# Kernel optimization log

Hardware: AMD Instinct MI355X
Metric: run time of the kernel (lower is better)

## Reference

```python
import jax, jax.numpy as jnp
import numpy as np

HID, H, C, L = 128, 4, 128, 3  # hidden, heads, per-head out (concat=False -> mean over heads), layers
OUT = 256
N_HEX, N_VERT, N_EDGE, B = 19, 54, 72, 1024
F_HEX, F_VERT, F_EDGE, F_PLY = 9, 7, 5, 14


def _topology():
    # Deterministic stand-in for the Catan board topology (same edge counts as the env).
    rng = np.random.RandomState(0)
    hv = rng.randint(0, N_VERT, size=(N_HEX, 6))            # each hex touches 6 vertices
    v0 = rng.randint(0, N_VERT, size=N_EDGE)                # board-edge endpoints
    v1 = (v0 + 1 + rng.randint(0, N_VERT - 1, size=N_EDGE)) % N_VERT
    h_src = np.repeat(np.arange(N_HEX), 6); h_dst = hv.reshape(-1)           # 114 edges
    e_src = np.repeat(np.arange(N_EDGE), 2); e_dst = np.stack([v0, v1], 1).reshape(-1)  # 144
    vv_s = np.concatenate([v0, v1]); vv_d = np.concatenate([v1, v0])          # 144
    # (src_idx, dst_idx, n_dst) per relation, order matches RELATION_TYPES
    rels = [(h_src, h_dst, N_VERT),   # hex -> vertex
            (h_dst, h_src, N_HEX),    # vertex -> hex
            (e_dst, e_src, N_EDGE),   # vertex -> edge
            (e_src, e_dst, N_VERT),   # edge -> vertex
            (vv_s, vv_d, N_VERT)]     # vertex -> vertex
    return [(jnp.asarray(s, jnp.int32), jnp.asarray(d, jnp.int32), nd) for s, d, nd in rels]

RELS = _topology()
REL_TYPES = [("hex", "vertex"), ("vertex", "hex"), ("vertex", "edge"), ("edge", "vertex"), ("vertex", "vertex")]
NODE_TYPES = ("hex", "vertex", "edge")


def _gat(x_src, x_dst, W, a_s, a_d, b, src, dst, n_dst):
    """PyG GATConv (heads=H, concat=False, add_self_loops=False, shared lin)."""
    bsz = x_src.shape[0]
    g = (x_src @ W).reshape(bsz, -1, H, C)    # [B,Ns,H,C]
    gd = (x_dst @ W).reshape(bsz, -1, H, C)   # [B,Nd,H,C]
    es = jnp.einsum('bnhc,hc->bnh', g, a_s)
    ed = jnp.einsum('bnhc,hc->bnh', gd, a_d)
    e = jax.nn.leaky_relu(es[:, src] + ed[:, dst], 0.2)   # [B,E,H]
    e = jnp.transpose(e, (1, 0, 2))                       # [E,B,H]
    m = jax.ops.segment_max(e, dst, num_segments=n_dst)   # per-dst softmax
    ex = jnp.exp(e - m[dst])
    s = jax.ops.segment_sum(ex, dst, num_segments=n_dst)
    alpha = ex / (s[dst] + 1e-16)
    msg = jnp.transpose(g, (1, 0, 2, 3))[src] * alpha[..., None]   # [E,B,H,C]
    out = jax.ops.segment_sum(msg, dst, num_segments=n_dst)       # [Nd,B,H,C]
    return jnp.transpose(out.mean(axis=2), (1, 0, 2)) + b         # mean over heads, + bias


def _ln(x, g, b):
    mu = x.mean(-1, keepdims=True)
    var = ((x - mu) ** 2).mean(-1, keepdims=True)
    return (x - mu) / jnp.sqrt(var + 1e-5) * g + b


def setup_inputs() -> dict:
    key = jax.random.key(0)
    ks = jax.random.split(key, 20)
    rn = lambda k, shape, s=0.05: jax.random.normal(k, shape, jnp.float32) * s
    pool_dim = 3 * HID + F_PLY
    return {
        'hex_features': rn(ks[0], (B, N_HEX, F_HEX), 1.0),
        'vertex_features': rn(ks[1], (B, N_VERT, F_VERT), 1.0),
        'edge_features': rn(ks[2], (B, N_EDGE, F_EDGE), 1.0),
        'player_features': rn(ks[3], (B, 4, F_PLY), 1.0),
        'in_hexW': rn(ks[4], (F_HEX, HID)), 'in_hexb': jnp.zeros((HID,), jnp.float32),
        'in_vertW': rn(ks[5], (F_VERT, HID)), 'in_vertb': jnp.zeros((HID,), jnp.float32),
        'in_edgeW': rn(ks[6], (F_EDGE, HID)), 'in_edgeb': jnp.zeros((HID,), jnp.float32),
        'gat_W': rn(ks[7], (L, 5, HID, H * C)),
        'gat_asrc': rn(ks[8], (L, 5, H, C)),
        'gat_adst': rn(ks[9], (L, 5, H, C)),
        'gat_b': jnp.zeros((L, 5, C), jnp.float32),
        'ln_g': jnp.ones((L, 3, HID), jnp.float32),
        'ln_b': jnp.zeros((L, 3, HID), jnp.float32),
        'mlp_W1': rn(ks[10], (pool_dim, HID)), 'mlp_b1': jnp.zeros((HID,), jnp.float32),
        'mlp_W2': rn(ks[11], (HID, OUT)), 'mlp_b2': jnp.zeros((OUT,), jnp.float32),
        'current_player': jax.random.randint(ks[12], (B,), 0, 4, jnp.int32),
    }


def reference(hex_features, vertex_features, edge_features, player_features,
              in_hexW, in_hexb, in_vertW, in_vertb, in_edgeW, in_edgeb,
              gat_W, gat_asrc, gat_adst, gat_b, ln_g, ln_b,
              mlp_W1, mlp_b1, mlp_W2, mlp_b2, current_player):
    x = {'hex': hex_features @ in_hexW + in_hexb,
         'vertex': vertex_features @ in_vertW + in_vertb,
         'edge': edge_features @ in_edgeW + in_edgeb}
    for l in range(L):
        agg = {nt: jnp.zeros_like(x[nt]) for nt in NODE_TYPES}
        for r, (st, dt) in enumerate(REL_TYPES):
            src, dst, n_dst = RELS[r]
            agg[dt] = agg[dt] + _gat(x[st], x[dt], gat_W[l, r], gat_asrc[l, r],
                                     gat_adst[l, r], gat_b[l, r], src, dst, n_dst)
        for i, nt in enumerate(NODE_TYPES):
            x[nt] = jax.nn.relu(_ln(agg[nt] + x[nt], ln_g[l, i], ln_b[l, i]))
    pools = [x[nt].mean(axis=1) for nt in NODE_TYPES]  # mean-pool each node type
    cur = jnp.take_along_axis(player_features, current_player[:, None, None], axis=1)[:, 0]
    feat = jnp.concatenate(pools + [cur], axis=-1)     # [B, 3*HID + F_PLY]
    h = jax.nn.relu(feat @ mlp_W1 + mlp_b1)
    return h @ mlp_W2 + mlp_b2
```

## Files before the change

### kernel.cpp

```cpp
#include <hip/hip_runtime.h>
#include <math.h>

#define NB 1024
#define NHEX 19
#define NVERT 54
#define NEDGE 72
#define NNODE 145
#define HID 128
#define NLAYERS 3
#define MAXE 144
#define OUTD 256
#define FPLY 14
#define POOLD 398

typedef unsigned short ushort_t;
typedef short bf16x8 __attribute__((ext_vector_type(8)));
typedef float f32x4 __attribute__((ext_vector_type(4)));
typedef float f32x2 __attribute__((ext_vector_type(2)));

static __device__ __forceinline__ float bf2f(ushort_t u) {
    return __uint_as_float(((unsigned int)u) << 16);
}
static __device__ __forceinline__ ushort_t f2bf(float f) {
    unsigned int u = __float_as_uint(f);
    return (ushort_t)((u + 0x7fffu + ((u >> 16) & 1u)) >> 16);
}
static __device__ __forceinline__ unsigned pk2(float lo, float hi) {
    unsigned r;
    asm("v_cvt_pk_bf16_f32 %0, %1, %2" : "=v"(r) : "v"(lo), "v"(hi));
    return r;
}
static __device__ __forceinline__ float blo(unsigned u) { return __uint_as_float(u << 16); }
static __device__ __forceinline__ float bhi(unsigned u) { return __uint_as_float(u & 0xffff0000u); }
static __device__ __forceinline__ f32x4 MF(uint4 a, uint4 b, f32x4 c) {
    return __builtin_amdgcn_mfma_f32_16x16x32_bf16(
        __builtin_bit_cast(bf16x8, a), __builtin_bit_cast(bf16x8, b), c, 0, 0, 0);
}

__device__ __forceinline__ void topo_body(int* __restrict__ cst_g, unsigned* __restrict__ pck_g) {
    __shared__ unsigned mt[624];
    __shared__ int t6[624];
    __shared__ int sc[624];
    __shared__ int hv[114], v0a[72], v1a[72];
    __shared__ int cnt[80];
    __shared__ int dloc[73 * 24];
    __shared__ int J186;
    const int tid = threadIdx.x;

    if (tid == 0) {
        unsigned s = 0u;
        for (int i = 0; i < 624; ++i) { mt[i] = s; s = 1812433253u * (s ^ (s >> 30)) + (unsigned)i + 1u; }
    }
    __syncthreads();
    {
        unsigned a = 0, bb = 0, c = 0;
        if (tid < 227) { a = mt[tid]; bb = mt[tid + 1]; c = mt[tid + 397]; }
        __syncthreads();
        if (tid < 227) {
            unsigned y = (a & 0x80000000u) | (bb & 0x7fffffffu);
            mt[tid] = c ^ (y >> 1) ^ ((bb & 1u) ? 0x9908b0dfu : 0u);
        }
        __syncthreads();
    }
    {
        int i = 227 + tid;
        unsigned a = 0, bb = 0, c = 0;
        if (tid < 227) { a = mt[i]; bb = mt[i + 1]; c = mt[i - 227]; }
        __syncthreads();
        if (tid < 227) {
            unsigned y = (a & 0x80000000u) | (bb & 0x7fffffffu);
            mt[i] = c ^ (y >> 1) ^ ((bb & 1u) ? 0x9908b0dfu : 0u);
        }
        __syncthreads();
    }
    {
        int i = 454 + tid;
        unsigned a = 0, bb = 0, c = 0;
        if (tid < 170) { a = mt[i]; bb = mt[(i + 1) % 624]; c = mt[i - 227]; }
        __syncthreads();
        if (tid < 170) {
            unsigned y = (a & 0x80000000u) | (bb & 0x7fffffffu);
            mt[i] = c ^ (y >> 1) ^ ((bb & 1u) ? 0x9908b0dfu : 0u);
        }
        __syncthreads();
    }
    for (int i = tid; i < 624; i += 256) {
        unsigned y = mt[i];
        y ^= y >> 11; y ^= (y << 7) & 0x9d2c5680u; y ^= (y << 15) & 0xefc60000u; y ^= y >> 18;
        t6[i] = (int)(y & 63u);
    }
    __syncthreads();
#define SCAN624()                                                          \
    for (int off = 1; off < 624; off <<= 1) {                              \
        int v0_ = 0, v1_ = 0, v2_ = 0;                                     \
        int i0 = tid, i1 = tid + 256, i2 = tid + 512;                      \
        if (i0 >= off) v0_ = sc[i0 - off];                                 \
        if (i1 >= off) v1_ = sc[i1 - off];                                 \
        if (i2 < 624 && i2 >= off) v2_ = sc[i2 - off];                     \
        __syncthreads();                                                   \
        sc[i0] += v0_; sc[i1] += v1_;                                      \
        if (i2 < 624) sc[i2] += v2_;                                       \
        __syncthreads();                                                   \
    }
    for (int i = tid; i < 624; i += 256) sc[i] = (t6[i] <= 53) ? 1 : 0;
    __syncthreads();
    SCAN624();
    for (int i = tid; i < 624; i += 256) {
        if (t6[i] <= 53) {
            int k = sc[i];
            if (k <= 114) hv[k - 1] = t6[i];
            else if (k <= 186) v0a[k - 115] = t6[i];
            if (k == 186) J186 = i;
        }
    }
    __syncthreads();
    int Jcap = J186;
    for (int i = tid; i < 624; i += 256) sc[i] = (i > Jcap && t6[i] <= 52) ? 1 : 0;
    __syncthreads();
    SCAN624();
    for (int i = tid; i < 624; i += 256) {
        if (i > Jcap && t6[i] <= 52) {
            int k = sc[i];
            if (k <= 72) v1a[k - 1] = (v0a[k - 1] + 1 + t6[i]) % 54;
        }
    }
    __syncthreads();
#undef SCAN624
    const int En[5] = {114, 114, 144, 144, 144};
    const int Ndn[5] = {54, 19, 72, 54, 54};
    for (int r = 0; r < 5; ++r) {
        int E = En[r], Nd = Ndn[r];
        int myc = 0;
        if (tid < Nd) {
            int* ss = dloc + tid * 24;
            for (int k = 0; k < E; ++k) {
                int s, d;
                if (r == 0)      { s = k / 6; d = hv[k]; }
                else if (r == 1) { s = hv[k]; d = k / 6; }
                else if (r == 2) { s = (k & 1) ? v1a[k >> 1] : v0a[k >> 1]; d = k >> 1; }
                else if (r == 3) { s = k >> 1; d = (k & 1) ? v1a[k >> 1] : v0a[k >> 1]; }
                else             { s = (k < 72) ? v0a[k] : v1a[k - 72]; d = (k < 72) ? v1a[k] : v0a[k - 72]; }
                if (d != tid) continue;
                int f = -1;
                for (int i2 = 0; i2 < myc; ++i2) if ((ss[i2] & 255) == s) { f = i2; break; }
                if (f >= 0) ss[f] += 1 << 16;
                else { if (myc < 24) { ss[myc++] = s | (1 << 16); } }
            }
            cnt[tid] = myc;
        }
        __syncthreads();
        for (int off = 1; off < 128; off <<= 1) {
            int v = 0;
            if (tid < Nd && tid >= off) v = cnt[tid - off];
            __syncthreads();
            if (tid < Nd && tid >= off) cnt[tid] += v;
            __syncthreads();
        }
        if (tid < Nd) {
            int st = cnt[tid] - myc;
            cst_g[r * 73 + tid] = st;
            if (tid == Nd - 1) cst_g[r * 73 + Nd] = cnt[tid];
            int* ss = dloc + tid * 24;
            for (int i2 = 0; i2 < myc; ++i2)
                pck_g[r * 144 + st + i2] =
                    (unsigned)((ss[i2] & 255) | (tid << 8) | ((ss[i2] >> 16) << 16));
        }
        __syncthreads();
    }
}

__device__ __forceinline__ void wvec_body(int lr, const float* __restrict__ gat_W,
                                          const float* __restrict__ gat_asrc,
                                          const float* __restrict__ gat_adst,
                                          ushort_t* __restrict__ wvb) {
    __shared__ float as_s[512], ad_s[512];
    int tid = threadIdx.x;
    for (int i = tid; i < 512; i += 256) {
        as_s[i] = gat_asrc[(size_t)lr * 512 + i];
        ad_s[i] = gat_adst[(size_t)lr * 512 + i];
    }
    __syncthreads();
    ushort_t* wb = wvb + (size_t)lr * 2048;
    const float* W = gat_W + (size_t)lr * 128 * 512;
    int t127 = tid & 127, rhalf = tid >> 7;
    int h = t127 >> 5, c4 = t127 & 31;
    for (int k0 = 0; k0 < 128; k0 += 2) {
        int k = k0 + rhalf;
        float4 wv4 = *(const float4*)(W + (size_t)k * 512 + h * 128 + c4 * 4);
        const float* a = as_s + h * 128 + c4 * 4;
        const float* dd = ad_s + h * 128 + c4 * 4;
        float pa = wv4.x * a[0] + wv4.y * a[1] + wv4.z * a[2] + wv4.w * a[3];
        float pd = wv4.x * dd[0] + wv4.y * dd[1] + wv4.z * dd[2] + wv4.w * dd[3];
        for (int m = 1; m < 32; m <<= 1) { pa += __shfl_xor(pa, m, 64); pd += __shfl_xor(pd, m, 64); }
        if (c4 == 0) {
            ushort_t pah = f2bf(pa), pdh = f2bf(pd);
            ushort_t pal = f2bf(pa - bf2f(pah)), pdl = f2bf(pd - bf2f(pdh));
            wb[h * 128 + k] = pah;        wb[(4 + h) * 128 + k] = pdh;
            wb[(8 + h) * 128 + k] = pal;  wb[(12 + h) * 128 + k] = pdl;
        }
    }
}

__device__ __forceinline__ void wp_body(int lrh, const float* __restrict__ gat_W, ushort_t* __restrict__ Wp) {
    __shared__ ushort_t tr[128 * 130];
    int lr = lrh >> 2, h = lrh & 3;
    const float* Wsrc = gat_W + (size_t)lr * 128 * 512 + h * 128;
    for (int i = threadIdx.x; i < 128 * 32; i += 256) {
        int k = i >> 5, q = i & 31;
        float4 v = *(const float4*)(Wsrc + (size_t)k * 512 + q * 4);
        int n = q * 4;
        tr[(n + 0) * 130 + k] = f2bf(v.x);
        tr[(n + 1) * 130 + k] = f2bf(v.y);
        tr[(n + 2) * 130 + k] = f2bf(v.z);
        tr[(n + 3) * 130 + k] = f2bf(v.w);
    }
    __syncthreads();
    ushort_t* dst = Wp + (size_t)lrh * 128 * 128;
    for (int i = threadIdx.x; i < 128 * 16; i += 256) {
        int n = i >> 4, q = i & 15;
        const ushort_t* s = tr + n * 130 + q * 8;
        uint4 o;
        o.x = (unsigned)s[0] | ((unsigned)s[1] << 16);
        o.y = (unsigned)s[2] | ((unsigned)s[3] << 16);
        o.z = (unsigned)s[4] | ((unsigned)s[5] << 16);
        o.w = (unsigned)s[6] | ((unsigned)s[7] << 16);
        *(uint4*)(dst + n * 128 + q * 8) = o;
    }
}

__device__ __forceinline__ void proj_body(int b, const float* __restrict__ hexf, const float* __restrict__ vertf,
                                          const float* __restrict__ edgef,
                                          const float* __restrict__ Wh, const float* __restrict__ bh,
                                          const float* __restrict__ Wv, const float* __restrict__ bv,
                                          const float* __restrict__ We, const float* __restrict__ be,
                                          ushort_t* __restrict__ xb) {
    __shared__ float Wl[(9 + 7 + 5) * 128];
    __shared__ float bl[3 * 128];
    int tid = threadIdx.x;
    for (int i = tid; i < 9 * 128; i += 256) Wl[i] = Wh[i];
    for (int i = tid; i < 7 * 128; i += 256) Wl[9 * 128 + i] = Wv[i];
    for (int i = tid; i < 5 * 128; i += 256) Wl[16 * 128 + i] = We[i];
    if (tid < 128) { bl[tid] = bh[tid]; bl[128 + tid] = bv[tid]; bl[256 + tid] = be[tid]; }
    __syncthreads();
    int c = tid & 127;
    for (int n = tid >> 7; n < NNODE; n += 2) {
        const float* f; const float* W; const float* bias; int K;
        if (n < NHEX)              { f = hexf  + ((size_t)b * NHEX  + n) * 9;                  W = Wl;            bias = bl;       K = 9; }
        else if (n < NHEX + NVERT) { f = vertf + ((size_t)b * NVERT + (n - NHEX)) * 7;         W = Wl + 9 * 128;  bias = bl + 128; K = 7; }
        else                       { f = edgef + ((size_t)b * NEDGE + (n - NHEX - NVERT)) * 5; W = Wl + 16 * 128; bias = bl + 256; K = 5; }
        float acc = bias[c];
        for (int k = 0; k < K; ++k) acc += f[k] * W[k * 128 + c];
        xb[((size_t)b * NNODE + n) * HID + c] = f2bf(acc);
    }
}

__global__ __launch_bounds__(256) void k_pre(
        int* __restrict__ cst_g, unsigned* __restrict__ pck_g,
        const float* __restrict__ gatW, const float* __restrict__ gatas,
        const float* __restrict__ gatad, ushort_t* __restrict__ wvb, ushort_t* __restrict__ Wp,
        const float* __restrict__ hexf, const float* __restrict__ vertf, const float* __restrict__ edgef,
        const float* __restrict__ Wh, const float* __restrict__ bh,
        const float* __restrict__ Wv, const float* __restrict__ bv,
        const float* __restrict__ We, const float* __restrict__ be,
        ushort_t* __restrict__ xb) {
    unsigned kb = blockIdx.x;
    if (kb == 0)       topo_body(cst_g, pck_g);
    else if (kb < 16)  wvec_body((int)kb - 1, gatW, gatas, gatad, wvb);
    else if (kb < 76)  wp_body((int)kb - 16, gatW, Wp);
    else               proj_body((int)kb - 76, hexf, vertf, edgef, Wh, bh, Wv, bv, We, be, xb);
}

template<int KIND>
__device__ __forceinline__ void gnn_body(char* smem, int b,
        const ushort_t* __restrict__ xb_cur, ushort_t* __restrict__ xb_nxt,
        const int* __restrict__ cst_all, const unsigned* __restrict__ pck_all,
        const ushort_t* __restrict__ wvb, const ushort_t* __restrict__ Wp_g,
        const float* __restrict__ gatb_g,
        const float* __restrict__ lg, const float* __restrict__ lb, int l) {
    constexpr int ND    = (KIND == 0 ? 19 : KIND == 1 ? 72 : 54);
    constexpr int DB    = (KIND == 0 ? 0 : KIND == 1 ? 73 : 19);
    constexpr int NSMAX = (KIND == 2 ? 72 : 54);
    constexpr int NRELF = (KIND == 2 ? 3 : 1);
    constexpr int MT    = (ND + 15) / 16;
    constexpr int O_Y   = (ND + NSMAX) * 256;
    constexpr int YSZ   = (KIND == 2 ? ND * 256 : 0);
    constexpr int O_ESD = O_Y + YSZ;
    constexpr int O_AL  = O_ESD + 4032;
    constexpr int O_CST = O_AL + 2304;
    constexpr int O_PCK = O_CST + 304;

    constexpr int NS_A[3][3] = {{54, 0, 0}, {54, 0, 0}, {19, 72, 54}};
    constexpr int SB_A[3][3] = {{19, 0, 0}, {19, 0, 0}, {0, 73, 19}};
    constexpr int RR_A[3][3] = {{1, 0, 0}, {2, 0, 0}, {0, 3, 4}};

    float*    esd  = (float*)(smem + O_ESD);
    float*    alph = (float*)(smem + O_AL);
    int*      cstL = (int*)(smem + O_CST);
    unsigned* pckL = (unsigned*)(smem + O_PCK);

    const int tid = threadIdx.x, lane = tid & 63, wid = tid >> 6;
    const int nr0 = wid * 32 + (lane & 15);
    const int kc16 = (lane >> 4) * 16;
    const ushort_t* xcb = xb_cur + (size_t)b * NNODE * HID;

#define XBA(row, cb) (((row) * 256 + (cb)) ^ (((row) & 7) << 4))
#define YBA(row, cb) ((KIND == 2 ? O_Y : 0) + ((((row) * 256) + (cb)) ^ (((row) & 7) << 4)))

    for (int i = tid; i < ND * 16; i += 256) {
        int row = i >> 4, q = i & 15;
        uint4 o = *(const uint4*)(xcb + (size_t)(DB + row) * HID + q * 8);
        *(uint4*)(smem + XBA(row, q * 16)) = o;
    }

    f32x4 acc[MT][2];
#pragma unroll
    for (int mt = 0; mt < MT; ++mt) {
        acc[mt][0] = (f32x4){0.f, 0.f, 0.f, 0.f};
        acc[mt][1] = (f32x4){0.f, 0.f, 0.f, 0.f};
    }

#pragma unroll
    for (int ri = 0; ri < NRELF; ++ri) {
        const int NS = NS_A[KIND][ri], SBG = SB_A[KIND][ri], r = RR_A[KIND][ri];
        const bool SELF = (KIND == 2 && ri == 2);
        const int RL = SELF ? ND : ND + NS;
        const int lr = l * 5 + r;

        if (!SELF)
            for (int i = tid; i < NS * 16; i += 256) {
                int row = ND + (i >> 4), q = i & 15;
                uint4 o = *(const uint4*)(xcb + (size_t)(SBG + (i >> 4)) * HID + q * 8);
                *(uint4*)(smem + XBA(row, q * 16)) = o;
            }
        for (int i = tid; i <= ND; i += 256) cstL[i] = cst_all[r * 73 + i];
        for (int i = tid; i < 144; i += 256) pckL[i] = pck_all[r * 144 + i];
        __syncthreads();

        {
            const ushort_t* wv = wvb + (size_t)lr * 2048;
            uint4 bw[4];
#pragma unroll
            for (int ks = 0; ks < 4; ++ks)
                bw[ks] = *(const uint4*)(wv + (lane & 15) * 128 + ks * 32 + (lane >> 4) * 8);
            const int T = (RL + 15) >> 4;
            for (int t = wid; t < T; t += 4) {
                f32x4 e = (f32x4){0.f, 0.f, 0.f, 0.f};
                int arow = t * 16 + (lane & 15);
#pragma unroll
                for (int ks = 0; ks < 4; ++ks) {
                    uint4 av = *(const uint4*)(smem + XBA(arow, ks * 64 + kc16));
                    e = MF(av, bw[ks], e);
                }
#pragma unroll
                for (int g = 0; g < 4; ++g) {
                    float sv = e[g] + __shfl_xor(e[g], 8, 64);
                    int row = t * 16 + (lane >> 4) * 4 + g;
                    if ((lane & 15) < 8 && row < RL) esd[row * 8 + (lane & 15)] = sv;
                }
            }
        }
        __syncthreads();

        for (int i = tid; i < ND * 4; i += 256) {
            int d = i >> 2, h = i & 3;
            int s0 = cstL[d], s1 = cstL[d + 1];
            if (s0 == s1) continue;
            float edv = esd[d * 8 + 4 + h];
            float m = -1e30f;
            for (int j = s0; j < s1; ++j) {
                int s = pckL[j] & 255;
                float sv = esd[(SELF ? s : ND + s) * 8 + h] + edv;
                sv = (sv >= 0.f) ? sv : 0.2f * sv;
                alph[j * 4 + h] = sv;
                m = fmaxf(m, sv);
            }
            float sum = 0.f;
            for (int j = s0; j < s1; ++j) {
                float e = (float)(pckL[j] >> 16) * __expf(alph[j * 4 + h] - m);
                alph[j * 4 + h] = e;
                sum += e;
            }
            float inv = 1.f / (sum + 1e-16f);
            for (int j = s0; j < s1; ++j) alph[j * 4 + h] *= inv;
        }
        __syncthreads();

        for (int h = 0; h < 4; ++h) {
            for (int i = tid; i < ND * 16; i += 256) {
                int d = i >> 4, c8 = i & 15;
                int s0 = cstL[d], s1 = cstL[d + 1];
                f32x2 a01 = (f32x2){0.f, 0.f}, a23 = (f32x2){0.f, 0.f};
                f32x2 a45 = (f32x2){0.f, 0.f}, a67 = (f32x2){0.f, 0.f};
                for (int j = s0; j < s1; ++j) {
                    float al = alph[j * 4 + h];
                    f32x2 al2 = (f32x2){al, al};
                    int s = pckL[j] & 255;
                    int srow = SELF ? s : ND + s;
                    uint4 xv = *(const uint4*)(smem + XBA(srow, c8 * 16));
                    a01 += al2 * (f32x2){blo(xv.x), bhi(xv.x)};
                    a23 += al2 * (f32x2){blo(xv.y), bhi(xv.y)};
                    a45 += al2 * (f32x2){blo(xv.z), bhi(xv.z)};
                    a67 += al2 * (f32x2){blo(xv.w), bhi(xv.w)};
                }
                uint4 o;
                o.x = pk2(a01[0], a01[1]); o.y = pk2(a23[0], a23[1]);
                o.z = pk2(a45[0], a45[1]); o.w = pk2(a67[0], a67[1]);
                *(uint4*)(smem + YBA(d, c8 * 16)) = o;
            }
            const ushort_t* wpH = Wp_g + (size_t)(lr * 4 + h) * 16384;
            uint4 bfr[8];
#pragma unroll
            for (int nt = 0; nt < 2; ++nt)
#pragma unroll
                for (int ks = 0; ks < 4; ++ks)
                    bfr[nt * 4 + ks] = *(const uint4*)(wpH + (size_t)(nr0 + nt * 16) * 128 + ks * 32 + (lane >> 4) * 8);
            __syncthreads();
#pragma unroll
            for (int ks = 0; ks < 4; ++ks)
#pragma unroll
                for (int mt = 0; mt < MT; ++mt) {
                    int arow = mt * 16 + (lane & 15);
                    if (arow >= ND) arow = ND - 1;
                    uint4 av = *(const uint4*)(smem + YBA(arow, ks * 64 + kc16));
                    acc[mt][0] = MF(av, bfr[ks], acc[mt][0]);
                    acc[mt][1] = MF(av, bfr[4 + ks], acc[mt][1]);
                }
            __syncthreads();
        }
    }

    float bn0 = 0.f, bn1 = 0.f;
#pragma unroll
    for (int ri = 0; ri < NRELF; ++ri) {
        const float* bb = gatb_g + (size_t)(l * 5 + RR_A[KIND][ri]) * 128;
        bn0 += bb[nr0]; bn1 += bb[nr0 + 16];
    }
    float* lnb_s = (float*)smem;
#pragma unroll
    for (int mt = 0; mt < MT; ++mt)
#pragma unroll
        for (int nt = 0; nt < 2; ++nt) {
            int n = nr0 + nt * 16;
            float bn = nt ? bn1 : bn0;
#pragma unroll
            for (int g = 0; g < 4; ++g) {
                int row = mt * 16 + (lane >> 4) * 4 + g;
                if (row < ND)
                    lnb_s[row * 128 + n] = 0.25f * acc[mt][nt][g] + bn
                        + bf2f(xcb[(size_t)(DB + row) * HID + n]);
            }
        }
    __syncthreads();
    for (int d = wid; d < ND; d += 4) {
        float a0 = lnb_s[d * 128 + lane];
        float a1 = lnb_s[d * 128 + 64 + lane];
        float s = a0 + a1;
        for (int m = 1; m < 64; m <<= 1) s += __shfl_xor(s, m, 64);
        float mu = s * (1.f / 128.f);
        float dv0 = a0 - mu, dv1 = a1 - mu;
        float q = dv0 * dv0 + dv1 * dv1;
        for (int m = 1; m < 64; m <<= 1) q += __shfl_xor(q, m, 64);
        float rs = rsqrtf(q * (1.f / 128.f) + 1e-5f);
        float o0 = fmaxf(dv0 * rs * lg[lane] + lb[lane], 0.f);
        float o1 = fmaxf(dv1 * rs * lg[64 + lane] + lb[64 + lane], 0.f);
        size_t gi = ((size_t)b * NNODE + DB + d) * 128;
        xb_nxt[gi + lane] = f2bf(o0);
        xb_nxt[gi + 64 + lane] = f2bf(o1);
    }
#undef XBA
#undef YBA
}

#define SMEM_TOT 53296

__global__ __launch_bounds__(256, 2) void k_layer(
        const ushort_t* __restrict__ xb_cur, ushort_t* __restrict__ xb_nxt,
        const int* __restrict__ cst, const unsigned* __restrict__ pck,
        const ushort_t* __restrict__ wvb, const ushort_t* __restrict__ Wp,
        const float* __restrict__ gatb, const float* __restrict__ lngp,
        const float* __restrict__ lnbp, int l) {
    extern __shared__ uint4 smem_u4[];
    char* smem = (char*)smem_u4;
    unsigned kb = blockIdx.x;
    if (kb < NB)
        gnn_body<2>(smem, (int)kb, xb_cur, xb_nxt, cst, pck, wvb, Wp, gatb,
                    lngp + (size_t)(l * 3 + 1) * 128, lnbp + (size_t)(l * 3 + 1) * 128, l);
    else if (kb < 2 * NB)
        gnn_body<1>(smem, (int)(kb - NB), xb_cur, xb_nxt, cst, pck, wvb, Wp, gatb,
                    lngp + (size_t)(l * 3 + 2) * 128, lnbp + (size_t)(l * 3 + 2) * 128, l);
    else
        gnn_body<0>(smem, (int)(kb - 2 * NB), xb_cur, xb_nxt, cst, pck, wvb, Wp, gatb,
                    lngp + (size_t)(l * 3 + 0) * 128, lnbp + (size_t)(l * 3 + 0) * 128, l);
}

__global__ __launch_bounds__(256) void k_head(const ushort_t* __restrict__ xb, const float* __restrict__ playerf,
                                              const int* __restrict__ curp,
                                              const float* __restrict__ W1, const float* __restrict__ b1,
                                              const float* __restrict__ W2, const float* __restrict__ b2,
                                              float* __restrict__ out) {
    __shared__ float fs[POOLD];
    __shared__ float ps[256];
    __shared__ float h1s[HID];
    int b = blockIdx.x, t = threadIdx.x;
    int c = t & 127, half = t >> 7;
    const ushort_t* xbb = xb + (size_t)b * NNODE * HID;
    float s0 = 0.f, s1 = 0.f, s2 = 0.f;
    for (int n = half; n < NHEX; n += 2)                    s0 += bf2f(xbb[n * HID + c]);
    for (int n = NHEX + half; n < NHEX + NVERT; n += 2)     s1 += bf2f(xbb[n * HID + c]);
    for (int n = NHEX + NVERT + half; n < NNODE; n += 2)    s2 += bf2f(xbb[n * HID + c]);
    ps[t] = s0; __syncthreads();
    if (half == 0) fs[c] = (ps[c] + ps[128 + c]) * (1.f / 19.f);
    __syncthreads(); ps[t] = s1; __syncthreads();
    if (half == 0) fs[128 + c] = (ps[c] + ps[128 + c]) * (1.f / 54.f);
    __syncthreads(); ps[t] = s2; __syncthreads();
    if (half == 0) fs[256 + c] = (ps[c] + ps[128 + c]) * (1.f / 72.f);
    if (t < FPLY) fs[384 + t] = playerf[((size_t)b * 4 + curp[b]) * FPLY + t];
    __syncthreads();
    float a = 0.f;
    int k0 = half * 199, k1 = half ? POOLD : 199;
    for (int k = k0; k < k1; ++k) a += fs[k] * W1[(size_t)k * HID + c];
    ps[t] = a; __syncthreads();
    if (half == 0) h1s[c] = fmaxf(b1[c] + ps[c] + ps[128 + c], 0.f);
    __syncthreads();
    float o = b2[t];
    for (int j = 0; j < HID; ++j) o += h1s[j] * W2[(size_t)j * OUTD + t];
    out[(size_t)b * OUTD + t] = o;
}

static constexpr size_t alignUp(size_t v) { return (v + 255) & ~(size_t)255; }
static constexpr size_t OFF_CST  = 0;
static constexpr size_t OFF_PCK  = alignUp(OFF_CST + 5 * 73 * 4);
static constexpr size_t OFF_WVB  = alignUp(OFF_PCK + 5 * 144 * 4);
static constexpr size_t OFF_WP   = alignUp(OFF_WVB + (size_t)15 * 16 * 128 * 2);
static constexpr size_t OFF_XA   = alignUp(OFF_WP + (size_t)15 * 4 * 128 * 128 * 2);
static constexpr size_t OFF_XB2  = alignUp(OFF_XA + (size_t)NB * NNODE * HID * 2);

extern "C" void kernel_launch(void* const* d_in, const int* in_sizes, int n_in,
                              void* d_out, int out_size, void* d_ws, size_t ws_size,
                              hipStream_t stream) {
    (void)in_sizes; (void)n_in; (void)out_size; (void)ws_size;
    const float* hexf   = (const float*)d_in[0];
    const float* vertf  = (const float*)d_in[1];
    const float* edgef  = (const float*)d_in[2];
    const float* playerf= (const float*)d_in[3];
    const float* inhW   = (const float*)d_in[4];
    const float* inhb   = (const float*)d_in[5];
    const float* invW   = (const float*)d_in[6];
    const float* invb   = (const float*)d_in[7];
    const float* ineW   = (const float*)d_in[8];
    const float* ineb   = (const float*)d_in[9];
    const float* gatW   = (const float*)d_in[10];
    const float* gatas  = (const float*)d_in[11];
    const float* gatad  = (const float*)d_in[12];
    const float* gatb   = (const float*)d_in[13];
    const float* lngp   = (const float*)d_in[14];
    const float* lnbp   = (const float*)d_in[15];
    const float* mW1    = (const float*)d_in[16];
    const float* mb1    = (const float*)d_in[17];
    const float* mW2    = (const float*)d_in[18];
    const float* mb2    = (const float*)d_in[19];
    const int*   curp   = (const int*)d_in[20];
    float* out = (float*)d_out;

    char* ws = (char*)d_ws;
    int* cst        = (int*)(ws + OFF_CST);
    unsigned* pck   = (unsigned*)(ws + OFF_PCK);
    ushort_t* wvb   = (ushort_t*)(ws + OFF_WVB);
    ushort_t* Wp    = (ushort_t*)(ws + OFF_WP);
    ushort_t* xbA   = (ushort_t*)(ws + OFF_XA);
    ushort_t* xbB   = (ushort_t*)(ws + OFF_XB2);

    k_pre<<<76 + NB, 256, 0, stream>>>(cst, pck, gatW, gatas, gatad, wvb, Wp,
                                       hexf, vertf, edgef, inhW, inhb, invW, invb, ineW, ineb, xbA);

    for (int l = 0; l < NLAYERS; ++l) {
        const ushort_t* cur = (l & 1) ? xbB : xbA;
        ushort_t* nxt = (l & 1) ? xbA : xbB;
        k_layer<<<3 * NB, 256, SMEM_TOT, stream>>>(cur, nxt, cst, pck, wvb, Wp, gatb, lngp, lnbp, l);
    }

    k_head<<<NB, 256, 0, stream>>>(xbB, playerf, curp, mW1, mb1, mW2, mb2, out);
}
```

Before: 918.7 us.

## Precompute next-layer attention logits in layer epilogue and shrink LDS footprint

Moves the per-relation attention logit computation (x·(W·a)) out of each layer's main body. Layer 0's logits now come from a new k_logits0 kernel, and each later layer's logits are produced in the previous layer's epilogue from the freshly normalized outputs, then stored in global scratch buffers. The layer no longer keeps destination rows resident in shared memory, and LayerNorm is computed from registers with cross-wave reductions instead of a full fp32 staging buffer. Together these cut LDS from about 53KB to about 39.5KB so launch bounds can allow 4 blocks per CU. The cost is an extra kernel launch, extra global traffic for the logit buffers, and duplicated logit MFMAs for rows shared across relations.

```diff
diff --git a/kernel.cpp b/kernel.cpp
--- a/kernel.cpp
+++ b/kernel.cpp
@@ -12,6 +12,7 @@
 #define OUTD 256
 #define FPLY 14
 #define POOLD 398
+#define ESD_PB 5120
 
 typedef unsigned short ushort_t;
 typedef short bf16x8 __attribute__((ext_vector_type(8)));
@@ -35,6 +36,9 @@
 static __device__ __forceinline__ f32x4 MF(uint4 a, uint4 b, f32x4 c) {
     return __builtin_amdgcn_mfma_f32_16x16x32_bf16(
         __builtin_bit_cast(bf16x8, a), __builtin_bit_cast(bf16x8, b), c, 0, 0, 0);
+}
+static __device__ __forceinline__ int xba(int row, int cb) {
+    return (row * 256 + cb) ^ ((row & 7) << 4);
 }
 
 __device__ __forceinline__ void topo_body(int* __restrict__ cst_g, unsigned* __restrict__ pck_g) {
@@ -270,9 +274,51 @@
     else               proj_body((int)kb - 76, hexf, vertf, edgef, Wh, bh, Wv, bv, We, be, xb);
 }
 
+__global__ __launch_bounds__(256, 2) void k_logits0(const ushort_t* __restrict__ xb,
+        const ushort_t* __restrict__ wvb, float* __restrict__ esd_g) {
+    __shared__ __align__(16) char smem[NNODE * 256];
+    int b = blockIdx.x, tid = threadIdx.x, lane = tid & 63, wid = tid >> 6;
+    const int kc16 = (lane >> 4) * 16;
+    const ushort_t* xcb = xb + (size_t)b * NNODE * HID;
+    for (int i = tid; i < NNODE * 16; i += 256) {
+        int row = i >> 4, q = i & 15;
+        uint4 o = *(const uint4*)(xcb + (size_t)row * HID + q * 8);
+        *(uint4*)(smem + xba(row, q * 16)) = o;
+    }
+    __syncthreads();
+    const int NsA[5] = {19, 54, 54, 72, 54}, SbA[5] = {0, 19, 19, 73, 19};
+    const int NdA[5] = {54, 19, 72, 54, 54}, DbA[5] = {19, 0, 73, 19, 19};
+    for (int r = 0; r < 5; ++r) {
+        int Ns = NsA[r];
+        int RL = (r == 4) ? 54 : Ns + NdA[r];
+        const ushort_t* wv = wvb + (size_t)r * 2048;
+        uint4 bw[4];
+#pragma unroll
+        for (int ks = 0; ks < 4; ++ks)
+            bw[ks] = *(const uint4*)(wv + (lane & 15) * 128 + ks * 32 + (lane >> 4) * 8);
+        int T = (RL + 15) >> 4;
+        for (int t = wid; t < T; t += 4) {
+            int vrow = t * 16 + (lane & 15);
+            int node = vrow < Ns ? SbA[r] + vrow : (vrow < RL ? DbA[r] + (vrow - Ns) : SbA[r]);
+            f32x4 e = (f32x4){0.f, 0.f, 0.f, 0.f};
+#pragma unroll
+            for (int ks = 0; ks < 4; ++ks)
+                e = MF(*(const uint4*)(smem + xba(node, ks * 64 + kc16)), bw[ks], e);
+#pragma unroll
+            for (int g = 0; g < 4; ++g) {
+                float sv = e[g] + __shfl_xor(e[g], 8, 64);
+                int row = t * 16 + (lane >> 4) * 4 + g;
+                if ((lane & 15) < 8 && row < RL)
+                    esd_g[(size_t)b * ESD_PB + r * 1024 + row * 8 + (lane & 15)] = sv;
+            }
+        }
+    }
+}
+
 template<int KIND>
 __device__ __forceinline__ void gnn_body(char* smem, int b,
         const ushort_t* __restrict__ xb_cur, ushort_t* __restrict__ xb_nxt,
+        const float* __restrict__ esd_cur, float* __restrict__ esd_nxt,
         const int* __restrict__ cst_all, const unsigned* __restrict__ pck_all,
         const ushort_t* __restrict__ wvb, const ushort_t* __restrict__ Wp_g,
         const float* __restrict__ gatb_g,
@@ -282,18 +328,20 @@
     constexpr int NSMAX = (KIND == 2 ? 72 : 54);
     constexpr int NRELF = (KIND == 2 ? 3 : 1);
     constexpr int MT    = (ND + 15) / 16;
-    constexpr int O_Y   = (ND + NSMAX) * 256;
-    constexpr int YSZ   = (KIND == 2 ? ND * 256 : 0);
-    constexpr int O_ESD = O_Y + YSZ;
-    constexpr int O_AL  = O_ESD + 4032;
+    constexpr int O_Y   = NSMAX * 256;
+    constexpr int O_ESD = O_Y + ND * 256;
+    constexpr int O_AL  = O_ESD + 4064;
     constexpr int O_CST = O_AL + 2304;
     constexpr int O_PCK = O_CST + 304;
 
     constexpr int NS_A[3][3] = {{54, 0, 0}, {54, 0, 0}, {19, 72, 54}};
     constexpr int SB_A[3][3] = {{19, 0, 0}, {19, 0, 0}, {0, 73, 19}};
     constexpr int RR_A[3][3] = {{1, 0, 0}, {2, 0, 0}, {0, 3, 4}};
-
-    float*    esd  = (float*)(smem + O_ESD);
+    constexpr int NRE = (KIND == 2 ? 5 : 2);
+    constexpr int RE_R[3][5] = {{0, 1, 0, 0, 0}, {2, 3, 0, 0, 0}, {0, 1, 2, 3, 4}};
+    constexpr int RE_B[3][5] = {{0, 54, 0, 0, 0}, {54, 0, 0, 0, 0}, {19, 0, 0, 72, 0}};
+
+    float*    esdL = (float*)(smem + O_ESD);
     float*    alph = (float*)(smem + O_AL);
     int*      cstL = (int*)(smem + O_CST);
     unsigned* pckL = (unsigned*)(smem + O_PCK);
@@ -303,15 +351,6 @@
     const int kc16 = (lane >> 4) * 16;
     const ushort_t* xcb = xb_cur + (size_t)b * NNODE * HID;
 
-#define XBA(row, cb) (((row) * 256 + (cb)) ^ (((row) & 7) << 4))
-#define YBA(row, cb) ((KIND == 2 ? O_Y : 0) + ((((row) * 256) + (cb)) ^ (((row) & 7) << 4)))
-
-    for (int i = tid; i < ND * 16; i += 256) {
-        int row = i >> 4, q = i & 15;
-        uint4 o = *(const uint4*)(xcb + (size_t)(DB + row) * HID + q * 8);
-        *(uint4*)(smem + XBA(row, q * 16)) = o;
-    }
-
     f32x4 acc[MT][2];
 #pragma unroll
     for (int mt = 0; mt < MT; ++mt) {
@@ -323,53 +362,31 @@
     for (int ri = 0; ri < NRELF; ++ri) {
         const int NS = NS_A[KIND][ri], SBG = SB_A[KIND][ri], r = RR_A[KIND][ri];
         const bool SELF = (KIND == 2 && ri == 2);
-        const int RL = SELF ? ND : ND + NS;
         const int lr = l * 5 + r;
-
-        if (!SELF)
-            for (int i = tid; i < NS * 16; i += 256) {
-                int row = ND + (i >> 4), q = i & 15;
-                uint4 o = *(const uint4*)(xcb + (size_t)(SBG + (i >> 4)) * HID + q * 8);
-                *(uint4*)(smem + XBA(row, q * 16)) = o;
-            }
+        const int ER = SELF ? ND : NS + ND;
+
+        for (int i = tid; i < NS * 16; i += 256) {
+            int row = i >> 4, q = i & 15;
+            uint4 o = *(const uint4*)(xcb + (size_t)(SBG + row) * HID + q * 8);
+            *(uint4*)(smem + xba(row, q * 16)) = o;
+        }
+        {
+            const float* eg = esd_cur + (size_t)b * ESD_PB + (size_t)r * 1024;
+            for (int i = tid; i < ER * 2; i += 256)
+                ((uint4*)esdL)[i] = ((const uint4*)eg)[i];
+        }
         for (int i = tid; i <= ND; i += 256) cstL[i] = cst_all[r * 73 + i];
         for (int i = tid; i < 144; i += 256) pckL[i] = pck_all[r * 144 + i];
-        __syncthreads();
-
-        {
-            const ushort_t* wv = wvb + (size_t)lr * 2048;
-            uint4 bw[4];
-#pragma unroll
-            for (int ks = 0; ks < 4; ++ks)
-                bw[ks] = *(const uint4*)(wv + (lane & 15) * 128 + ks * 32 + (lane >> 4) * 8);
-            const int T = (RL + 15) >> 4;
-            for (int t = wid; t < T; t += 4) {
-                f32x4 e = (f32x4){0.f, 0.f, 0.f, 0.f};
-                int arow = t * 16 + (lane & 15);
-#pragma unroll
-                for (int ks = 0; ks < 4; ++ks) {
-                    uint4 av = *(const uint4*)(smem + XBA(arow, ks * 64 + kc16));
-                    e = MF(av, bw[ks], e);
-                }
-#pragma unroll
-                for (int g = 0; g < 4; ++g) {
-                    float sv = e[g] + __shfl_xor(e[g], 8, 64);
-                    int row = t * 16 + (lane >> 4) * 4 + g;
-                    if ((lane & 15) < 8 && row < RL) esd[row * 8 + (lane & 15)] = sv;
-                }
-            }
-        }
         __syncthreads();
 
         for (int i = tid; i < ND * 4; i += 256) {
             int d = i >> 2, h = i & 3;
             int s0 = cstL[d], s1 = cstL[d + 1];
             if (s0 == s1) continue;
-            float edv = esd[d * 8 + 4 + h];
+            float edv = esdL[(SELF ? d : NS + d) * 8 + 4 + h];
             float m = -1e30f;
             for (int j = s0; j < s1; ++j) {
-                int s = pckL[j] & 255;
-                float sv = esd[(SELF ? s : ND + s) * 8 + h] + edv;
+                float sv = esdL[(pckL[j] & 255) * 8 + h] + edv;
                 sv = (sv >= 0.f) ? sv : 0.2f * sv;
                 alph[j * 4 + h] = sv;
                 m = fmaxf(m, sv);
@@ -394,9 +411,7 @@
                 for (int j = s0; j < s1; ++j) {
                     float al = alph[j * 4 + h];
                     f32x2 al2 = (f32x2){al, al};
-                    int s = pckL[j] & 255;
-                    int srow = SELF ? s : ND + s;
-                    uint4 xv = *(const uint4*)(smem + XBA(srow, c8 * 16));
+                    uint4 xv = *(const uint4*)(smem + xba((int)(pckL[j] & 255), c8 * 16));
                     a01 += al2 * (f32x2){blo(xv.x), bhi(xv.x)};
                     a23 += al2 * (f32x2){blo(xv.y), bhi(xv.y)};
                     a45 += al2 * (f32x2){blo(xv.z), bhi(xv.z)};
@@ -405,7 +420,7 @@
                 uint4 o;
                 o.x = pk2(a01[0], a01[1]); o.y = pk2(a23[0], a23[1]);
                 o.z = pk2(a45[0], a45[1]); o.w = pk2(a67[0], a67[1]);
-                *(uint4*)(smem + YBA(d, c8 * 16)) = o;
+                *(uint4*)(smem + O_Y + xba(d, c8 * 16)) = o;
             }
             const ushort_t* wpH = Wp_g + (size_t)(lr * 4 + h) * 16384;
             uint4 bfr[8];
@@ -421,7 +436,7 @@
                 for (int mt = 0; mt < MT; ++mt) {
                     int arow = mt * 16 + (lane & 15);
                     if (arow >= ND) arow = ND - 1;
-                    uint4 av = *(const uint4*)(smem + YBA(arow, ks * 64 + kc16));
+                    uint4 av = *(const uint4*)(smem + O_Y + xba(arow, ks * 64 + kc16));
                     acc[mt][0] = MF(av, bfr[ks], acc[mt][0]);
                     acc[mt][1] = MF(av, bfr[4 + ks], acc[mt][1]);
                 }
@@ -435,46 +450,98 @@
         const float* bb = gatb_g + (size_t)(l * 5 + RR_A[KIND][ri]) * 128;
         bn0 += bb[nr0]; bn1 += bb[nr0 + 16];
     }
-    float* lnb_s = (float*)smem;
+    const float lgc0 = lg[nr0], lgc1 = lg[nr0 + 16];
+    const float lbc0 = lb[nr0], lbc1 = lb[nr0 + 16];
 #pragma unroll
     for (int mt = 0; mt < MT; ++mt)
 #pragma unroll
-        for (int nt = 0; nt < 2; ++nt) {
-            int n = nr0 + nt * 16;
-            float bn = nt ? bn1 : bn0;
+        for (int g = 0; g < 4; ++g) {
+            int row = mt * 16 + (lane >> 4) * 4 + g;
+            if (row < ND) {
+                acc[mt][0][g] = 0.25f * acc[mt][0][g] + bn0 + bf2f(xcb[(size_t)(DB + row) * HID + nr0]);
+                acc[mt][1][g] = 0.25f * acc[mt][1][g] + bn1 + bf2f(xcb[(size_t)(DB + row) * HID + nr0 + 16]);
+            }
+        }
+    float* red1 = esdL;
+    float* red2 = esdL + 320;
+#pragma unroll
+    for (int mt = 0; mt < MT; ++mt)
+#pragma unroll
+        for (int g = 0; g < 4; ++g) {
+            float p = acc[mt][0][g] + acc[mt][1][g];
+            for (int m = 1; m < 16; m <<= 1) p += __shfl_xor(p, m, 64);
+            int row = mt * 16 + (lane >> 4) * 4 + g;
+            if ((lane & 15) == 0 && row < ND) red1[row * 4 + wid] = p;
+        }
+    __syncthreads();
+    float mu[MT][4];
+#pragma unroll
+    for (int mt = 0; mt < MT; ++mt)
+#pragma unroll
+        for (int g = 0; g < 4; ++g) {
+            int row = mt * 16 + (lane >> 4) * 4 + g;
+            mu[mt][g] = 0.f;
+            if (row < ND)
+                mu[mt][g] = (red1[row * 4] + red1[row * 4 + 1] + red1[row * 4 + 2] + red1[row * 4 + 3]) * (1.f / 128.f);
+            float d0 = acc[mt][0][g] - mu[mt][g], d1 = acc[mt][1][g] - mu[mt][g];
+            float p = d0 * d0 + d1 * d1;
+            for (int m = 1; m < 16; m <<= 1) p += __shfl_xor(p, m, 64);
+            if ((lane & 15) == 0 && row < ND) red2[row * 4 + wid] = p;
+        }
+    __syncthreads();
+#pragma unroll
+    for (int mt = 0; mt < MT; ++mt)
+#pragma unroll
+        for (int g = 0; g < 4; ++g) {
+            int row = mt * 16 + (lane >> 4) * 4 + g;
+            if (row < ND) {
+                float var = (red2[row * 4] + red2[row * 4 + 1] + red2[row * 4 + 2] + red2[row * 4 + 3]) * (1.f / 128.f);
+                float rs = rsqrtf(var + 1e-5f);
+                float o0 = fmaxf((acc[mt][0][g] - mu[mt][g]) * rs * lgc0 + lbc0, 0.f);
+                float o1 = fmaxf((acc[mt][1][g] - mu[mt][g]) * rs * lgc1 + lbc1, 0.f);
+                size_t gi = ((size_t)b * NNODE + DB + row) * HID;
+                ushort_t u0 = f2bf(o0), u1 = f2bf(o1);
+                xb_nxt[gi + nr0] = u0;
+                xb_nxt[gi + nr0 + 16] = u1;
+                if (esd_nxt) {
+                    *(ushort_t*)(smem + O_Y + xba(row, nr0 * 2)) = u0;
+                    *(ushort_t*)(smem + O_Y + xba(row, (nr0 + 16) * 2)) = u1;
+                }
+            }
+        }
+    if (esd_nxt) {
+        __syncthreads();
+        const int T = (ND + 15) >> 4;
+        for (int t5 = wid; t5 < NRE * T; t5 += 4) {
+            int e = t5 / T, tt = t5 % T;
+            int r2 = RE_R[KIND][e], base = RE_B[KIND][e];
+            const ushort_t* wv = wvb + (size_t)((l + 1) * 5 + r2) * 2048;
+            uint4 bw[4];
+#pragma unroll
+            for (int ks = 0; ks < 4; ++ks)
+                bw[ks] = *(const uint4*)(wv + (lane & 15) * 128 + ks * 32 + (lane >> 4) * 8);
+            int arow = tt * 16 + (lane & 15);
+            if (arow >= ND) arow = ND - 1;
+            f32x4 ev = (f32x4){0.f, 0.f, 0.f, 0.f};
+#pragma unroll
+            for (int ks = 0; ks < 4; ++ks)
+                ev = MF(*(const uint4*)(smem + O_Y + xba(arow, ks * 64 + kc16)), bw[ks], ev);
 #pragma unroll
             for (int g = 0; g < 4; ++g) {
-                int row = mt * 16 + (lane >> 4) * 4 + g;
-                if (row < ND)
-                    lnb_s[row * 128 + n] = 0.25f * acc[mt][nt][g] + bn
-                        + bf2f(xcb[(size_t)(DB + row) * HID + n]);
-            }
-        }
-    __syncthreads();
-    for (int d = wid; d < ND; d += 4) {
-        float a0 = lnb_s[d * 128 + lane];
-        float a1 = lnb_s[d * 128 + 64 + lane];
-        float s = a0 + a1;
-        for (int m = 1; m < 64; m <<= 1) s += __shfl_xor(s, m, 64);
-        float mu = s * (1.f / 128.f);
-        float dv0 = a0 - mu, dv1 = a1 - mu;
-        float q = dv0 * dv0 + dv1 * dv1;
-        for (int m = 1; m < 64; m <<= 1) q += __shfl_xor(q, m, 64);
-        float rs = rsqrtf(q * (1.f / 128.f) + 1e-5f);
-        float o0 = fmaxf(dv0 * rs * lg[lane] + lb[lane], 0.f);
-        float o1 = fmaxf(dv1 * rs * lg[64 + lane] + lb[64 + lane], 0.f);
-        size_t gi = ((size_t)b * NNODE + DB + d) * 128;
-        xb_nxt[gi + lane] = f2bf(o0);
-        xb_nxt[gi + 64 + lane] = f2bf(o1);
-    }
-#undef XBA
-#undef YBA
-}
-
-#define SMEM_TOT 53296
-
-__global__ __launch_bounds__(256, 2) void k_layer(
+                float sv = ev[g] + __shfl_xor(ev[g], 8, 64);
+                int row = tt * 16 + (lane >> 4) * 4 + g;
+                if ((lane & 15) < 8 && row < ND)
+                    esd_nxt[(size_t)b * ESD_PB + r2 * 1024 + (base + row) * 8 + (lane & 15)] = sv;
+            }
+        }
+    }
+}
+
+#define SMEM_TOT 39504
+
+__global__ __launch_bounds__(256, 4) void k_layer(
         const ushort_t* __restrict__ xb_cur, ushort_t* __restrict__ xb_nxt,
+        const float* __restrict__ esd_cur, float* __restrict__ esd_nxt,
         const int* __restrict__ cst, const unsigned* __restrict__ pck,
         const ushort_t* __restrict__ wvb, const ushort_t* __restrict__ Wp,
         const float* __restrict__ gatb, const float* __restrict__ lngp,
@@ -483,13 +550,13 @@
     char* smem = (char*)smem_u4;
     unsigned kb = blockIdx.x;
     if (kb < NB)
-        gnn_body<2>(smem, (int)kb, xb_cur, xb_nxt, cst, pck, wvb, Wp, gatb,
+        gnn_body<2>(smem, (int)kb, xb_cur, xb_nxt, esd_cur, esd_nxt, cst, pck, wvb, Wp, gatb,
                     lngp + (size_t)(l * 3 + 1) * 128, lnbp + (size_t)(l * 3 + 1) * 128, l);
     else if (kb < 2 * NB)
-        gnn_body<1>(smem, (int)(kb - NB), xb_cur, xb_nxt, cst, pck, wvb, Wp, gatb,
+        gnn_body<1>(smem, (int)(kb - NB), xb_cur, xb_nxt, esd_cur, esd_nxt, cst, pck, wvb, Wp, gatb,
                     lngp + (size_t)(l * 3 + 2) * 128, lnbp + (size_t)(l * 3 + 2) * 128, l);
     else
-        gnn_body<0>(smem, (int)(kb - 2 * NB), xb_cur, xb_nxt, cst, pck, wvb, Wp, gatb,
+        gnn_body<0>(smem, (int)(kb - 2 * NB), xb_cur, xb_nxt, esd_cur, esd_nxt, cst, pck, wvb, Wp, gatb,
                     lngp + (size_t)(l * 3 + 0) * 128, lnbp + (size_t)(l * 3 + 0) * 128, l);
 }
 
@@ -534,6 +601,8 @@
 static constexpr size_t OFF_WP   = alignUp(OFF_WVB + (size_t)15 * 16 * 128 * 2);
 static constexpr size_t OFF_XA   = alignUp(OFF_WP + (size_t)15 * 4 * 128 * 128 * 2);
 static constexpr size_t OFF_XB2  = alignUp(OFF_XA + (size_t)NB * NNODE * HID * 2);
+static constexpr size_t OFF_ESD0 = alignUp(OFF_XB2 + (size_t)NB * NNODE * HID * 2);
+static constexpr size_t OFF_ESD1 = alignUp(OFF_ESD0 + (size_t)NB * ESD_PB * 4);
 
 extern "C" void kernel_launch(void* const* d_in, const int* in_sizes, int n_in,
                               void* d_out, int out_size, void* d_ws, size_t ws_size,
@@ -569,14 +638,20 @@
     ushort_t* Wp    = (ushort_t*)(ws + OFF_WP);
     ushort_t* xbA   = (ushort_t*)(ws + OFF_XA);
     ushort_t* xbB   = (ushort_t*)(ws + OFF_XB2);
+    float* esd0     = (float*)(ws + OFF_ESD0);
+    float* esd1     = (float*)(ws + OFF_ESD1);
 
     k_pre<<<76 + NB, 256, 0, stream>>>(cst, pck, gatW, gatas, gatad, wvb, Wp,
                                        hexf, vertf, edgef, inhW, inhb, invW, invb, ineW, ineb, xbA);
+    k_logits0<<<NB, 256, 0, stream>>>(xbA, wvb, esd0);
 
     for (int l = 0; l < NLAYERS; ++l) {
         const ushort_t* cur = (l & 1) ? xbB : xbA;
         ushort_t* nxt = (l & 1) ? xbA : xbB;
-        k_layer<<<3 * NB, 256, SMEM_TOT, stream>>>(cur, nxt, cst, pck, wvb, Wp, gatb, lngp, lnbp, l);
+        const float* ecur = (l & 1) ? esd1 : esd0;
+        float* enxt = (l == 2) ? nullptr : ((l & 1) ? esd0 : esd1);
+        k_layer<<<3 * NB, 256, SMEM_TOT, stream>>>(cur, nxt, ecur, enxt, cst, pck, wvb, Wp,
+                                                   gatb, lngp, lnbp, l);
     }
 
     k_head<<<NB, 256, 0, stream>>>(xbB, playerf, curp, mW1, mb1, mW2, mb2, out);
```

Result: no change. 931.9 us (+1.4%).
